# Performance work log

Hardware: AMD Instinct MI355X
Metric: run time of the kernel (lower is better)

## Reference

```python
import jax, jax.numpy as jnp
import numpy as np

IN_DIM = 256
OUT_DIM = 256
BS = 8
NODE = 256
BN_EPS = 1e-5


def setup_inputs() -> dict:
    key = jax.random.key(0)
    ks = jax.random.split(key, 9)
    s_in = 1.0 / np.sqrt(IN_DIM)
    return {
        "x": jax.random.normal(ks[0], (BS, NODE, IN_DIM), dtype=jnp.float32),
        # att_proj: Linear(in_dim, out_dim)
        "Wp": jax.random.uniform(ks[1], (IN_DIM, OUT_DIM), jnp.float32, -s_in, s_in),
        "bp": jax.random.uniform(ks[2], (OUT_DIM,), jnp.float32, -s_in, s_in),
        # att_weight: (out_dim, 1) xavier_normal -> keep as (out_dim,)
        "w_att": jax.random.normal(ks[3], (OUT_DIM,), jnp.float32) * np.sqrt(2.0 / (OUT_DIM + 1)),
        # proj_with_att: Linear(in_dim, out_dim)
        "W1": jax.random.uniform(ks[4], (IN_DIM, OUT_DIM), jnp.float32, -s_in, s_in),
        "b1": jax.random.uniform(ks[5], (OUT_DIM,), jnp.float32, -s_in, s_in),
        # proj_without_att: Linear(in_dim, out_dim)
        "W2": jax.random.uniform(ks[6], (IN_DIM, OUT_DIM), jnp.float32, -s_in, s_in),
        "b2": jax.random.uniform(ks[7], (OUT_DIM,), jnp.float32, -s_in, s_in),
        # BatchNorm1d affine params
        "gamma": jnp.ones((OUT_DIM,), jnp.float32),
        "beta": jnp.zeros((OUT_DIM,), jnp.float32),
    }


def reference(x, Wp, bp, w_att, W1, b1, W2, b2, gamma, beta):
    # dropout is identity in eval mode
    # pairwise mult + att_proj fused: (b,n,m,do) = (x_n * x_m) @ Wp + bp
    h = jnp.tanh(jnp.einsum('bnd,bmd,de->bnme', x, x, Wp) + bp)
    scores = jnp.einsum('bnme,e->bnm', h, w_att)          # (b, n, m)
    att = jax.nn.softmax(scores, axis=1)                  # softmax over dim=-2 of (b,n,m,1) => axis n
    agg = jnp.einsum('bnm,bmd->bnd', att, x)              # att_map.squeeze(-1) @ x
    out = (agg @ W1 + b1) + (x @ W2 + b2)                 # dual projection
    # BatchNorm1d over flattened (bs*node) batch axis (training-mode batch stats)
    flat = out.reshape(-1, out.shape[-1])
    mean = jnp.mean(flat, axis=0)
    var = jnp.var(flat, axis=0)
    out = (out - mean) * jax.lax.rsqrt(var + BN_EPS) * gamma + beta
    return jax.nn.selu(out)
```

## Files before the change

kernel.cpp:

```cpp
#include <hip/hip_runtime.h>
#include <hip/hip_bf16.h>
#include <stdint.h>

using f32x16 = __attribute__((ext_vector_type(16))) float;
using short8 = __attribute__((ext_vector_type(8))) short;

#define C2LOG2E 2.8853900817779268f

static __device__ __forceinline__ unsigned cvt_pk_bf16(float lo, float hi) {
  unsigned r;
  asm("v_cvt_pk_bf16_f32 %0, %1, %2" : "=v"(r) : "v"(lo), "v"(hi));
  return r;
}

__device__ static const unsigned kMagicDiv[9] = {0u, 65536u, 32768u, 21846u, 16384u,
                                                 13108u, 10923u, 9363u, 8192u};

__global__ __launch_bounds__(256) void k_prep(const float* __restrict__ x,
                                              const float* __restrict__ Wp,
                                              unsigned int* __restrict__ xfrag,
                                              unsigned int* __restrict__ wpfrag) {
  const int bid = blockIdx.x, t = threadIdx.x;
  const int half = t >> 7, dpair = (t >> 5) & 3, rc = t & 31;
  const int kk = half * 8 + dpair * 2;
  if (bid < 1024) {
    const int b = bid >> 7, mt = (bid >> 4) & 7, ks = bid & 15;
    const int m = mt * 32 + rc;
    const int k = ks * 16 + kk;
    float2 v = *(const float2*)(x + (size_t)(b * 256 + m) * 256 + k);
    xfrag[(size_t)b * 32768 + ((mt * 16 + ks) << 8) + half * 128 + rc * 4 + dpair] =
        cvt_pk_bf16(v.x, v.y);
  } else {
    const int b2 = bid - 1024;
    const int et = b2 >> 4, ks = b2 & 15;
    const int e = et * 32 + rc;
    const int k = ks * 16 + kk;
    float v0 = Wp[(size_t)k * 256 + e];
    float v1 = Wp[(size_t)(k + 1) * 256 + e];
    wpfrag[((et * 16 + ks) << 8) + half * 128 + rc * 4 + dpair] = cvt_pk_bf16(v0, v1);
  }
}

__global__ __launch_bounds__(256, 2) void k_scores(
    const unsigned int* __restrict__ xfrag, const unsigned int* __restrict__ wpfrag,
    const float* __restrict__ bp, const float* __restrict__ watt,
    float* __restrict__ sp) {
  __shared__ unsigned char wplds[65536];

  const int tid = threadIdx.x;
  const int l = tid & 63, w = tid >> 6;
  const int c = l & 31, hi = l >> 5;
  const int h = blockIdx.x & 1;

  {
    const unsigned char* src = (const unsigned char*)wpfrag + (size_t)h * 65536;
    #pragma unroll
    for (int it = 0; it < 16; ++it) {
      __builtin_amdgcn_global_load_lds(
          (const __attribute__((address_space(1))) unsigned int*)(src + it * 4096 + w * 1024 + l * 16),
          (__attribute__((address_space(3))) unsigned int*)(&wplds[it * 4096 + w * 1024]),
          16, 0, 0);
    }
  }

  float bpe[4], wm2[4], Wl = 0.f;
  #pragma unroll
  for (int et = 0; et < 4; ++et) {
    float bv = bp[h * 128 + et * 32 + c];
    float wv = watt[h * 128 + et * 32 + c];
    bpe[et] = bv * C2LOG2E;
    wm2[et] = -2.f * wv;
    Wl += wv;
  }
  __syncthreads();

  const int gw = (blockIdx.x >> 1) * 4 + w;

  for (int i = gw; i < 9216; i += 1024) {
    int b = i / 1152;
    int r = i - b * 1152;
    int nt, cum;
    if      (r < 256)  { nt = 0; cum = 0; }
    else if (r < 480)  { nt = 1; cum = 256; }
    else if (r < 672)  { nt = 2; cum = 480; }
    else if (r < 832)  { nt = 3; cum = 672; }
    else if (r < 960)  { nt = 4; cum = 832; }
    else if (r < 1056) { nt = 5; cum = 960; }
    else               { nt = (r < 1120) ? 6 : 7; cum = (r < 1120) ? 1056 : 1120; }
    int rr = r - cum;
    int w8 = 8 - nt;
    int q0 = (int)(((unsigned)rr * kMagicDiv[w8]) >> 16);
    int n  = nt * 32 + q0;
    int mt = nt + (rr - q0 * w8);
    const int m0 = mt * 32;

    const unsigned char* xfb = (const unsigned char*)xfrag + (size_t)b * 131072;
    const unsigned char* xnbase = xfb + (nt << 14) + hi * 512 + q0 * 16;
    const unsigned char* xmbase = xfb + (mt << 14) + l * 16;

    f32x16 acc0, acc1, acc2, acc3;
    #pragma unroll
    for (int q = 0; q < 16; ++q) { acc0[q] = 0.f; acc1[q] = 0.f; acc2[q] = 0.f; acc3[q] = 0.f; }

    #pragma unroll 4
    for (int ks = 0; ks < 16; ++ks) {
      uint4 xnp = *(const uint4*)(xnbase + (ks << 10));
      uint4 xm  = *(const uint4*)(xmbase + (ks << 10));
      union U { uint4 u; short8 s; __hip_bfloat162 hh[4]; } a, mm, nn;
      mm.u = xm; nn.u = xnp;
      #pragma unroll
      for (int d = 0; d < 4; ++d) a.hh[d] = __hmul2(mm.hh[d], nn.hh[d]);

      short8 b0 = *(const short8*)(&wplds[((0 * 16 + ks) << 10) + l * 16]);
      short8 b1 = *(const short8*)(&wplds[((1 * 16 + ks) << 10) + l * 16]);
      short8 b2 = *(const short8*)(&wplds[((2 * 16 + ks) << 10) + l * 16]);
      short8 b3 = *(const short8*)(&wplds[((3 * 16 + ks) << 10) + l * 16]);
      acc0 = __builtin_amdgcn_mfma_f32_32x32x16_bf16(a.s, b0, acc0, 0, 0, 0);
      acc1 = __builtin_amdgcn_mfma_f32_32x32x16_bf16(a.s, b1, acc1, 0, 0, 0);
      acc2 = __builtin_amdgcn_mfma_f32_32x32x16_bf16(a.s, b2, acc2, 0, 0, 0);
      acc3 = __builtin_amdgcn_mfma_f32_32x32x16_bf16(a.s, b3, acc3, 0, 0, 0);
    }

    float p[16];
    #pragma unroll
    for (int q = 0; q < 16; ++q) {
      float v0 = fmaf(acc0[q], C2LOG2E, bpe[0]);
      float pq = fmaf(wm2[0], __builtin_amdgcn_rcpf(1.f + exp2f(v0)), Wl);
      float v1 = fmaf(acc1[q], C2LOG2E, bpe[1]);
      pq = fmaf(wm2[1], __builtin_amdgcn_rcpf(1.f + exp2f(v1)), pq);
      float v2 = fmaf(acc2[q], C2LOG2E, bpe[2]);
      pq = fmaf(wm2[2], __builtin_amdgcn_rcpf(1.f + exp2f(v2)), pq);
      float v3 = fmaf(acc3[q], C2LOG2E, bpe[3]);
      pq = fmaf(wm2[3], __builtin_amdgcn_rcpf(1.f + exp2f(v3)), pq);
      p[q] = pq;
    }

    #pragma unroll
    for (int q = 0; q < 16; ++q) {
      float v = p[q];
      v += __shfl_xor(v, 1);
      v += __shfl_xor(v, 2);
      v += __shfl_xor(v, 4);
      v += __shfl_xor(v, 8);
      v += __shfl_xor(v, 16);
      p[q] = v;
    }
    if (c == 0) {
      float* base = sp + (size_t)h * 524288;
      float* outrow = base + (size_t)(b * 256 + n) * 256 + m0;
      #pragma unroll
      for (int q = 0; q < 16; ++q) {
        int mr = (q & 3) + 8 * (q >> 2) + 4 * hi;
        outrow[mr] = p[q];
      }
      if (mt > nt) {
        #pragma unroll
        for (int q = 0; q < 16; ++q) {
          int mr = (q & 3) + 8 * (q >> 2) + 4 * hi;
          base[(size_t)(b * 256 + m0 + mr) * 256 + n] = p[q];
        }
      }
    }
  }
}

__global__ __launch_bounds__(256) void k_softmax(float* __restrict__ sp) {
  __shared__ float tile[256][65];
  __shared__ float red[4][64];
  const int t = threadIdx.x;
  const int bb = blockIdx.x >> 2, mt = blockIdx.x & 3;
  const int m0 = mt * 64;

  for (int c = 0; c < 64; ++c) {
    int nn = c * 4 + (t >> 6);
    size_t idx = (size_t)(bb * 256 + nn) * 256 + m0 + (t & 63);
    tile[nn][t & 63] = sp[idx] + sp[524288 + idx];
  }
  __syncthreads();
  const int col = t & 63, g = t >> 6;
  float mx = -1e30f;
  for (int k2 = 0; k2 < 64; ++k2) mx = fmaxf(mx, tile[g * 64 + k2][col]);
  red[g][col] = mx;
  __syncthreads();
  float M = fmaxf(fmaxf(red[0][col], red[1][col]), fmaxf(red[2][col], red[3][col]));
  float sm = 0.f;
  for (int k2 = 0; k2 < 64; ++k2) {
    float ev = __expf(tile[g * 64 + k2][col] - M);
    tile[g * 64 + k2][col] = ev;
    sm += ev;
  }
  __syncthreads();
  red[g][col] = sm;
  __syncthreads();
  float inv = 1.0f / (red[0][col] + red[1][col] + red[2][col] + red[3][col]);
  for (int k2 = 0; k2 < 64; ++k2) tile[g * 64 + k2][col] *= inv;
  __syncthreads();
  for (int c = 0; c < 64; ++c) {
    int nn = c * 4 + (t >> 6);
    sp[(size_t)(bb * 256 + nn) * 256 + m0 + (t & 63)] = tile[nn][t & 63];
  }
}

__global__ __launch_bounds__(256) void k_aggproj(
    const float* __restrict__ x, const float* __restrict__ att,
    const float* __restrict__ W1, const float* __restrict__ b1,
    const float* __restrict__ W2, const float* __restrict__ b2,
    float* __restrict__ out, float* __restrict__ bnpart) {
  __shared__ float att8[8][256];
  __shared__ float xn8[8][256];
  __shared__ float agg8[8][256];
  const int t = threadIdx.x;
  const int bb = blockIdx.x >> 5, ng = blockIdx.x & 31;
  const int n0 = ng * 8;

  #pragma unroll
  for (int i = 0; i < 8; ++i) {
    att8[i][t] = att[(size_t)(bb * 256 + n0 + i) * 256 + t];
    xn8[i][t]  = x  [(size_t)(bb * 256 + n0 + i) * 256 + t];
  }
  __syncthreads();

  float ar[8] = {0.f, 0.f, 0.f, 0.f, 0.f, 0.f, 0.f, 0.f};
  for (int m4 = 0; m4 < 64; ++m4) {
    int m = m4 * 4;
    float xv0 = x[(size_t)(bb * 256 + m + 0) * 256 + t];
    float xv1 = x[(size_t)(bb * 256 + m + 1) * 256 + t];
    float xv2 = x[(size_t)(bb * 256 + m + 2) * 256 + t];
    float xv3 = x[(size_t)(bb * 256 + m + 3) * 256 + t];
    #pragma unroll
    for (int i = 0; i < 8; ++i) {
      float4 av = *(const float4*)&att8[i][m];
      ar[i] += av.x * xv0 + av.y * xv1 + av.z * xv2 + av.w * xv3;
    }
  }
  #pragma unroll
  for (int i = 0; i < 8; ++i) agg8[i][t] = ar[i];
  __syncthreads();

  float o[8];
  float bsum = b1[t] + b2[t];
  #pragma unroll
  for (int i = 0; i < 8; ++i) o[i] = bsum;
  for (int d4 = 0; d4 < 64; ++d4) {
    int d = d4 * 4;
    float w10 = W1[(d + 0) * 256 + t], w11 = W1[(d + 1) * 256 + t];
    float w12 = W1[(d + 2) * 256 + t], w13 = W1[(d + 3) * 256 + t];
    float w20 = W2[(d + 0) * 256 + t], w21 = W2[(d + 1) * 256 + t];
    float w22 = W2[(d + 2) * 256 + t], w23 = W2[(d + 3) * 256 + t];
    #pragma unroll
    for (int i = 0; i < 8; ++i) {
      float4 ag = *(const float4*)&agg8[i][d];
      float4 xn = *(const float4*)&xn8[i][d];
      o[i] += ag.x * w10 + ag.y * w11 + ag.z * w12 + ag.w * w13
            + xn.x * w20 + xn.y * w21 + xn.z * w22 + xn.w * w23;
    }
  }
  float s1 = 0.f, s2 = 0.f;
  #pragma unroll
  for (int i = 0; i < 8; ++i) {
    out[(size_t)(bb * 256 + n0 + i) * 256 + t] = o[i];
    s1 += o[i];
    s2 += o[i] * o[i];
  }
  bnpart[(size_t)blockIdx.x * 512 + t]       = s1;
  bnpart[(size_t)blockIdx.x * 512 + 256 + t] = s2;
}

__global__ __launch_bounds__(256) void k_bnstats(const float* __restrict__ bnpart,
                                                 float* __restrict__ bnacc) {
  __shared__ float r4[4];
  const int s = blockIdx.x;
  const int t = threadIdx.x;
  float v = bnpart[(size_t)t * 512 + s];
  v += __shfl_xor(v, 1);
  v += __shfl_xor(v, 2);
  v += __shfl_xor(v, 4);
  v += __shfl_xor(v, 8);
  v += __shfl_xor(v, 16);
  v += __shfl_xor(v, 32);
  if ((t & 63) == 0) r4[t >> 6] = v;
  __syncthreads();
  if (t == 0) bnacc[s] = r4[0] + r4[1] + r4[2] + r4[3];
}

__global__ __launch_bounds__(256) void k_bnapply(float* __restrict__ io,
                                                 const float* __restrict__ bnacc,
                                                 const float* __restrict__ gamma,
                                                 const float* __restrict__ beta) {
  const int e = threadIdx.x;
  float mean = bnacc[e] * (1.0f / 2048.0f);
  float var  = bnacc[256 + e] * (1.0f / 2048.0f) - mean * mean;
  float scl  = rsqrtf(var + 1e-5f) * gamma[e];
  float sh   = beta[e] - mean * scl;
  for (int r = blockIdx.x; r < 2048; r += gridDim.x) {
    float v = io[(size_t)r * 256 + e];
    float y = v * scl + sh;
    float s = (y > 0.f) ? 1.0507009873554805f * y
                        : 1.7580993408473766f * (__expf(y) - 1.0f);
    io[(size_t)r * 256 + e] = s;
  }
}

extern "C" void kernel_launch(void* const* d_in, const int* in_sizes, int n_in,
                              void* d_out, int out_size, void* d_ws, size_t ws_size,
                              hipStream_t stream) {
  const float* x     = (const float*)d_in[0];
  const float* Wp    = (const float*)d_in[1];
  const float* bp    = (const float*)d_in[2];
  const float* watt  = (const float*)d_in[3];
  const float* W1    = (const float*)d_in[4];
  const float* b1    = (const float*)d_in[5];
  const float* W2    = (const float*)d_in[6];
  const float* b2    = (const float*)d_in[7];
  const float* gamma = (const float*)d_in[8];
  const float* beta  = (const float*)d_in[9];
  float* out = (float*)d_out;
  float* ws  = (float*)d_ws;

  float* sp = ws;
  unsigned int* wpfragG = (unsigned int*)(ws + 1048576);
  unsigned int* xfragG  = wpfragG + 32768;
  float* bnpart = ws + 524288;
  float* bnacc  = bnpart + 131072;

  k_prep   <<<1152, 256, 0, stream>>>(x, Wp, xfragG, wpfragG);
  k_scores <<<512,  256, 0, stream>>>(xfragG, wpfragG, bp, watt, sp);
  k_softmax<<<32,   256, 0, stream>>>(sp);
  k_aggproj<<<256,  256, 0, stream>>>(x, sp, W1, b1, W2, b2, out, bnpart);
  k_bnstats<<<512,  256, 0, stream>>>(bnpart, bnacc);
  k_bnapply<<<256,  256, 0, stream>>>(out, bnacc, gamma, beta);
}
```

Baseline: 129.8 us.

## Split score projection over four output-dim quarters and use DPP for lane reductions

The pairwise score kernel now splits the output dimension into four 64-wide quarters instead of two 128-wide halves. This doubles the grid, halves the per-block LDS weight tile and halves the accumulator registers per wave, so more waves can be resident. The softmax kernel now sums four partial score planes, and the workspace offsets move to fit the larger partial buffer. In exchange, each x_n*x_m product and its global loads are recomputed twice as often, and partial-score store and read traffic doubles. Separately, the first four xor-shuffle reduction steps are replaced with DPP row operations to cut cross-lane shuffle cost.

After: 159.2 us. 1.23x slower.

```diff
diff --git a/kernel.cpp b/kernel.cpp
--- a/kernel.cpp
+++ b/kernel.cpp
@@ -12,6 +12,16 @@
   asm("v_cvt_pk_bf16_f32 %0, %1, %2" : "=v"(r) : "v"(lo), "v"(hi));
   return r;
 }
+
+template <int CTRL>
+static __device__ __forceinline__ float dpp_add(float v) {
+  int x = __builtin_amdgcn_update_dpp(0, __float_as_int(v), CTRL, 0xF, 0xF, true);
+  return v + __int_as_float(x);
+}
+#define DPP_XOR1 0xB1
+#define DPP_XOR2 0x4E
+#define DPP_XOR4 0x141
+#define DPP_XOR8 0x140
 
 __device__ static const unsigned kMagicDiv[9] = {0u, 65536u, 32768u, 21846u, 16384u,
                                                  13108u, 10923u, 9363u, 8192u};
@@ -45,17 +55,17 @@
     const unsigned int* __restrict__ xfrag, const unsigned int* __restrict__ wpfrag,
     const float* __restrict__ bp, const float* __restrict__ watt,
     float* __restrict__ sp) {
-  __shared__ unsigned char wplds[65536];
+  __shared__ unsigned char wplds[32768];
 
   const int tid = threadIdx.x;
   const int l = tid & 63, w = tid >> 6;
   const int c = l & 31, hi = l >> 5;
-  const int h = blockIdx.x & 1;
+  const int h = blockIdx.x & 3;
 
   {
-    const unsigned char* src = (const unsigned char*)wpfrag + (size_t)h * 65536;
-    #pragma unroll
-    for (int it = 0; it < 16; ++it) {
+    const unsigned char* src = (const unsigned char*)wpfrag + (size_t)h * 32768;
+    #pragma unroll
+    for (int it = 0; it < 8; ++it) {
       __builtin_amdgcn_global_load_lds(
           (const __attribute__((address_space(1))) unsigned int*)(src + it * 4096 + w * 1024 + l * 16),
           (__attribute__((address_space(3))) unsigned int*)(&wplds[it * 4096 + w * 1024]),
@@ -63,18 +73,18 @@
     }
   }
 
-  float bpe[4], wm2[4], Wl = 0.f;
-  #pragma unroll
-  for (int et = 0; et < 4; ++et) {
-    float bv = bp[h * 128 + et * 32 + c];
-    float wv = watt[h * 128 + et * 32 + c];
+  float bpe[2], wm2[2], Wl = 0.f;
+  #pragma unroll
+  for (int et = 0; et < 2; ++et) {
+    float bv = bp[h * 64 + et * 32 + c];
+    float wv = watt[h * 64 + et * 32 + c];
     bpe[et] = bv * C2LOG2E;
     wm2[et] = -2.f * wv;
     Wl += wv;
   }
   __syncthreads();
 
-  const int gw = (blockIdx.x >> 1) * 4 + w;
+  const int gw = (blockIdx.x >> 2) * 4 + w;
 
   for (int i = gw; i < 9216; i += 1024) {
     int b = i / 1152;
@@ -98,9 +108,9 @@
     const unsigned char* xnbase = xfb + (nt << 14) + hi * 512 + q0 * 16;
     const unsigned char* xmbase = xfb + (mt << 14) + l * 16;
 
-    f32x16 acc0, acc1, acc2, acc3;
-    #pragma unroll
-    for (int q = 0; q < 16; ++q) { acc0[q] = 0.f; acc1[q] = 0.f; acc2[q] = 0.f; acc3[q] = 0.f; }
+    f32x16 acc0, acc1;
+    #pragma unroll
+    for (int q = 0; q < 16; ++q) { acc0[q] = 0.f; acc1[q] = 0.f; }
 
     #pragma unroll 4
     for (int ks = 0; ks < 16; ++ks) {
@@ -113,12 +123,8 @@
 
       short8 b0 = *(const short8*)(&wplds[((0 * 16 + ks) << 10) + l * 16]);
       short8 b1 = *(const short8*)(&wplds[((1 * 16 + ks) << 10) + l * 16]);
-      short8 b2 = *(const short8*)(&wplds[((2 * 16 + ks) << 10) + l * 16]);
-      short8 b3 = *(const short8*)(&wplds[((3 * 16 + ks) << 10) + l * 16]);
       acc0 = __builtin_amdgcn_mfma_f32_32x32x16_bf16(a.s, b0, acc0, 0, 0, 0);
       acc1 = __builtin_amdgcn_mfma_f32_32x32x16_bf16(a.s, b1, acc1, 0, 0, 0);
-      acc2 = __builtin_amdgcn_mfma_f32_32x32x16_bf16(a.s, b2, acc2, 0, 0, 0);
-      acc3 = __builtin_amdgcn_mfma_f32_32x32x16_bf16(a.s, b3, acc3, 0, 0, 0);
     }
 
     float p[16];
@@ -128,20 +134,16 @@
       float pq = fmaf(wm2[0], __builtin_amdgcn_rcpf(1.f + exp2f(v0)), Wl);
       float v1 = fmaf(acc1[q], C2LOG2E, bpe[1]);
       pq = fmaf(wm2[1], __builtin_amdgcn_rcpf(1.f + exp2f(v1)), pq);
-      float v2 = fmaf(acc2[q], C2LOG2E, bpe[2]);
-      pq = fmaf(wm2[2], __builtin_amdgcn_rcpf(1.f + exp2f(v2)), pq);
-      float v3 = fmaf(acc3[q], C2LOG2E, bpe[3]);
-      pq = fmaf(wm2[3], __builtin_amdgcn_rcpf(1.f + exp2f(v3)), pq);
       p[q] = pq;
     }
 
     #pragma unroll
     for (int q = 0; q < 16; ++q) {
       float v = p[q];
-      v += __shfl_xor(v, 1);
-      v += __shfl_xor(v, 2);
-      v += __shfl_xor(v, 4);
-      v += __shfl_xor(v, 8);
+      v = dpp_add<DPP_XOR1>(v);
+      v = dpp_add<DPP_XOR2>(v);
+      v = dpp_add<DPP_XOR4>(v);
+      v = dpp_add<DPP_XOR8>(v);
       v += __shfl_xor(v, 16);
       p[q] = v;
     }
@@ -174,7 +176,7 @@
   for (int c = 0; c < 64; ++c) {
     int nn = c * 4 + (t >> 6);
     size_t idx = (size_t)(bb * 256 + nn) * 256 + m0 + (t & 63);
-    tile[nn][t & 63] = sp[idx] + sp[524288 + idx];
+    tile[nn][t & 63] = sp[idx] + sp[524288 + idx] + sp[1048576 + idx] + sp[1572864 + idx];
   }
   __syncthreads();
   const int col = t & 63, g = t >> 6;
@@ -318,13 +320,13 @@
   float* ws  = (float*)d_ws;
 
   float* sp = ws;
-  unsigned int* wpfragG = (unsigned int*)(ws + 1048576);
+  unsigned int* wpfragG = (unsigned int*)(ws + 2097152);
   unsigned int* xfragG  = wpfragG + 32768;
   float* bnpart = ws + 524288;
-  float* bnacc  = bnpart + 131072;
+  float* bnacc  = (float*)(xfragG + 262144);
 
   k_prep   <<<1152, 256, 0, stream>>>(x, Wp, xfragG, wpfragG);
-  k_scores <<<512,  256, 0, stream>>>(xfragG, wpfragG, bp, watt, sp);
+  k_scores <<<1024, 256, 0, stream>>>(xfragG, wpfragG, bp, watt, sp);
   k_softmax<<<32,   256, 0, stream>>>(sp);
   k_aggproj<<<256,  256, 0, stream>>>(x, sp, W1, b1, W2, b2, out, bnpart);
   k_bnstats<<<512,  256, 0, stream>>>(bnpart, bnacc);
```

## Compute two score rows per wave and use DPP for lane reductions

Applied to the files above, without the earlier changes.

Each wave in the scores kernel now produces two n rows (n and n+16) for the same m tile. The xm fragment and the four Wp LDS fragments are loaded once and feed eight MFMA accumulators instead of four, which halves the number of work items and the repeated loads. The first four butterfly steps of the cross-lane reduction use DPP row permutes in place of ds_swizzle/shuffle. Launch bounds drop to one block per SIMD pair so the doubled accumulators fit in registers, which costs occupancy and latency hiding.

Result: slower. 169.2 us (+30.3%).

```diff
diff --git a/kernel.cpp b/kernel.cpp
--- a/kernel.cpp
+++ b/kernel.cpp
@@ -12,6 +12,16 @@
   asm("v_cvt_pk_bf16_f32 %0, %1, %2" : "=v"(r) : "v"(lo), "v"(hi));
   return r;
 }
+
+template <int CTRL>
+static __device__ __forceinline__ float dpp_add(float v) {
+  int x = __builtin_amdgcn_update_dpp(0, __float_as_int(v), CTRL, 0xF, 0xF, true);
+  return v + __int_as_float(x);
+}
+#define DPP_XOR1 0xB1
+#define DPP_XOR2 0x4E
+#define DPP_XOR4 0x141
+#define DPP_XOR8 0x140
 
 __device__ static const unsigned kMagicDiv[9] = {0u, 65536u, 32768u, 21846u, 16384u,
                                                  13108u, 10923u, 9363u, 8192u};
@@ -41,7 +51,7 @@
   }
 }
 
-__global__ __launch_bounds__(256, 2) void k_scores(
+__global__ __launch_bounds__(256, 1) void k_scores(
     const unsigned int* __restrict__ xfrag, const unsigned int* __restrict__ wpfrag,
     const float* __restrict__ bp, const float* __restrict__ watt,
     float* __restrict__ sp) {
@@ -76,88 +86,107 @@
 
   const int gw = (blockIdx.x >> 1) * 4 + w;
 
-  for (int i = gw; i < 9216; i += 1024) {
-    int b = i / 1152;
-    int r = i - b * 1152;
+  for (int i = gw; i < 4608; i += 1024) {
+    int b = (int)((((unsigned)i >> 6) * 7282u) >> 16);
+    int r = i - b * 576;
     int nt, cum;
-    if      (r < 256)  { nt = 0; cum = 0; }
-    else if (r < 480)  { nt = 1; cum = 256; }
-    else if (r < 672)  { nt = 2; cum = 480; }
-    else if (r < 832)  { nt = 3; cum = 672; }
-    else if (r < 960)  { nt = 4; cum = 832; }
-    else if (r < 1056) { nt = 5; cum = 960; }
-    else               { nt = (r < 1120) ? 6 : 7; cum = (r < 1120) ? 1056 : 1120; }
+    if      (r < 128) { nt = 0; cum = 0; }
+    else if (r < 240) { nt = 1; cum = 128; }
+    else if (r < 336) { nt = 2; cum = 240; }
+    else if (r < 416) { nt = 3; cum = 336; }
+    else if (r < 480) { nt = 4; cum = 416; }
+    else if (r < 528) { nt = 5; cum = 480; }
+    else              { nt = (r < 560) ? 6 : 7; cum = (r < 560) ? 528 : 560; }
     int rr = r - cum;
-    int w8 = 8 - nt;
-    int q0 = (int)(((unsigned)rr * kMagicDiv[w8]) >> 16);
-    int n  = nt * 32 + q0;
-    int mt = nt + (rr - q0 * w8);
+    int d8 = 8 - nt;
+    int q0 = (int)(((unsigned)rr * kMagicDiv[d8]) >> 16);
+    int mt = nt + (rr - q0 * d8);
+    const int n1 = nt * 32 + q0, n2 = n1 + 16;
     const int m0 = mt * 32;
 
     const unsigned char* xfb = (const unsigned char*)xfrag + (size_t)b * 131072;
-    const unsigned char* xnbase = xfb + (nt << 14) + hi * 512 + q0 * 16;
-    const unsigned char* xmbase = xfb + (mt << 14) + l * 16;
-
-    f32x16 acc0, acc1, acc2, acc3;
-    #pragma unroll
-    for (int q = 0; q < 16; ++q) { acc0[q] = 0.f; acc1[q] = 0.f; acc2[q] = 0.f; acc3[q] = 0.f; }
+    const unsigned char* xmb = xfb + (mt << 14) + l * 16;
+    const unsigned char* xnb = xfb + (nt << 14) + hi * 512 + q0 * 16;
+
+    f32x16 a10, a11, a12, a13, a20, a21, a22, a23;
+    #pragma unroll
+    for (int q = 0; q < 16; ++q) {
+      a10[q] = 0.f; a11[q] = 0.f; a12[q] = 0.f; a13[q] = 0.f;
+      a20[q] = 0.f; a21[q] = 0.f; a22[q] = 0.f; a23[q] = 0.f;
+    }
 
     #pragma unroll 4
     for (int ks = 0; ks < 16; ++ks) {
-      uint4 xnp = *(const uint4*)(xnbase + (ks << 10));
-      uint4 xm  = *(const uint4*)(xmbase + (ks << 10));
-      union U { uint4 u; short8 s; __hip_bfloat162 hh[4]; } a, mm, nn;
-      mm.u = xm; nn.u = xnp;
+      uint4 xm = *(const uint4*)(xmb + (ks << 10));
+      uint4 x1 = *(const uint4*)(xnb + (ks << 10));
+      uint4 x2 = *(const uint4*)(xnb + (ks << 10) + 256);
+      union U { uint4 u; short8 s; __hip_bfloat162 hh[4]; } m, u1, u2, p1, p2;
+      m.u = xm; u1.u = x1; u2.u = x2;
       #pragma unroll
-      for (int d = 0; d < 4; ++d) a.hh[d] = __hmul2(mm.hh[d], nn.hh[d]);
-
+      for (int dd = 0; dd < 4; ++dd) {
+        p1.hh[dd] = __hmul2(m.hh[dd], u1.hh[dd]);
+        p2.hh[dd] = __hmul2(m.hh[dd], u2.hh[dd]);
+      }
       short8 b0 = *(const short8*)(&wplds[((0 * 16 + ks) << 10) + l * 16]);
       short8 b1 = *(const short8*)(&wplds[((1 * 16 + ks) << 10) + l * 16]);
       short8 b2 = *(const short8*)(&wplds[((2 * 16 + ks) << 10) + l * 16]);
       short8 b3 = *(const short8*)(&wplds[((3 * 16 + ks) << 10) + l * 16]);
-      acc0 = __builtin_amdgcn_mfma_f32_32x32x16_bf16(a.s, b0, acc0, 0, 0, 0);
-      acc1 = __builtin_amdgcn_mfma_f32_32x32x16_bf16(a.s, b1, acc1, 0, 0, 0);
-      acc2 = __builtin_amdgcn_mfma_f32_32x32x16_bf16(a.s, b2, acc2, 0, 0, 0);
-      acc3 = __builtin_amdgcn_mfma_f32_32x32x16_bf16(a.s, b3, acc3, 0, 0, 0);
-    }
-
-    float p[16];
-    #pragma unroll
-    for (int q = 0; q < 16; ++q) {
-      float v0 = fmaf(acc0[q], C2LOG2E, bpe[0]);
-      float pq = fmaf(wm2[0], __builtin_amdgcn_rcpf(1.f + exp2f(v0)), Wl);
-      float v1 = fmaf(acc1[q], C2LOG2E, bpe[1]);
-      pq = fmaf(wm2[1], __builtin_amdgcn_rcpf(1.f + exp2f(v1)), pq);
-      float v2 = fmaf(acc2[q], C2LOG2E, bpe[2]);
-      pq = fmaf(wm2[2], __builtin_amdgcn_rcpf(1.f + exp2f(v2)), pq);
-      float v3 = fmaf(acc3[q], C2LOG2E, bpe[3]);
-      pq = fmaf(wm2[3], __builtin_amdgcn_rcpf(1.f + exp2f(v3)), pq);
-      p[q] = pq;
-    }
-
-    #pragma unroll
-    for (int q = 0; q < 16; ++q) {
-      float v = p[q];
-      v += __shfl_xor(v, 1);
-      v += __shfl_xor(v, 2);
-      v += __shfl_xor(v, 4);
-      v += __shfl_xor(v, 8);
-      v += __shfl_xor(v, 16);
-      p[q] = v;
-    }
-    if (c == 0) {
-      float* base = sp + (size_t)h * 524288;
-      float* outrow = base + (size_t)(b * 256 + n) * 256 + m0;
+      a10 = __builtin_amdgcn_mfma_f32_32x32x16_bf16(p1.s, b0, a10, 0, 0, 0);
+      a11 = __builtin_amdgcn_mfma_f32_32x32x16_bf16(p1.s, b1, a11, 0, 0, 0);
+      a12 = __builtin_amdgcn_mfma_f32_32x32x16_bf16(p1.s, b2, a12, 0, 0, 0);
+      a13 = __builtin_amdgcn_mfma_f32_32x32x16_bf16(p1.s, b3, a13, 0, 0, 0);
+      a20 = __builtin_amdgcn_mfma_f32_32x32x16_bf16(p2.s, b0, a20, 0, 0, 0);
+      a21 = __builtin_amdgcn_mfma_f32_32x32x16_bf16(p2.s, b1, a21, 0, 0, 0);
+      a22 = __builtin_amdgcn_mfma_f32_32x32x16_bf16(p2.s, b2, a22, 0, 0, 0);
+      a23 = __builtin_amdgcn_mfma_f32_32x32x16_bf16(p2.s, b3, a23, 0, 0, 0);
+    }
+
+    #pragma unroll
+    for (int nn = 0; nn < 2; ++nn) {
+      f32x16 c0 = nn ? a20 : a10;
+      f32x16 c1 = nn ? a21 : a11;
+      f32x16 c2 = nn ? a22 : a12;
+      f32x16 c3 = nn ? a23 : a13;
+      const int n = nn ? n2 : n1;
+
+      float p[16];
       #pragma unroll
       for (int q = 0; q < 16; ++q) {
-        int mr = (q & 3) + 8 * (q >> 2) + 4 * hi;
-        outrow[mr] = p[q];
+        float v0 = fmaf(c0[q], C2LOG2E, bpe[0]);
+        float pq = fmaf(wm2[0], __builtin_amdgcn_rcpf(1.f + exp2f(v0)), Wl);
+        float v1 = fmaf(c1[q], C2LOG2E, bpe[1]);
+        pq = fmaf(wm2[1], __builtin_amdgcn_rcpf(1.f + exp2f(v1)), pq);
+        float v2 = fmaf(c2[q], C2LOG2E, bpe[2]);
+        pq = fmaf(wm2[2], __builtin_amdgcn_rcpf(1.f + exp2f(v2)), pq);
+        float v3 = fmaf(c3[q], C2LOG2E, bpe[3]);
+        pq = fmaf(wm2[3], __builtin_amdgcn_rcpf(1.f + exp2f(v3)), pq);
+        p[q] = pq;
       }
-      if (mt > nt) {
+
+      #pragma unroll
+      for (int q = 0; q < 16; ++q) {
+        float v = p[q];
+        v = dpp_add<DPP_XOR1>(v);
+        v = dpp_add<DPP_XOR2>(v);
+        v = dpp_add<DPP_XOR4>(v);
+        v = dpp_add<DPP_XOR8>(v);
+        v += __shfl_xor(v, 16);
+        p[q] = v;
+      }
+      if (c == 0) {
+        float* base = sp + (size_t)h * 524288;
+        float* outrow = base + (size_t)(b * 256 + n) * 256 + m0;
         #pragma unroll
         for (int q = 0; q < 16; ++q) {
           int mr = (q & 3) + 8 * (q >> 2) + 4 * hi;
-          base[(size_t)(b * 256 + m0 + mr) * 256 + n] = p[q];
+          outrow[mr] = p[q];
+        }
+        if (mt > nt) {
+          #pragma unroll
+          for (int q = 0; q < 16; ++q) {
+            int mr = (q & 3) + 8 * (q >> 2) + 4 * hi;
+            base[(size_t)(b * 256 + m0 + mr) * 256 + n] = p[q];
+          }
         }
       }
     }
```
